# Kernel tuning notes

Hardware: AMD Instinct MI355X
Metric: run time of the kernel (lower is better)

The kernel has to match this reference:

```python
import jax, jax.numpy as jnp
import numpy as np

B, N, C = 16, 1024, 768
E, H, D, K = 8, 192, 4, 2


def setup_inputs() -> dict:
    key = jax.random.key(0)
    ks = jax.random.split(key, 8)
    std = 0.02
    return {
        "x": jax.random.normal(ks[0], (B, N, C), jnp.float32),
        "task_ids": jax.random.randint(ks[1], (B,), 0, D),
        "eps": jax.random.normal(ks[2], (B, N, E), jnp.float32),
        "gate_w": jax.random.normal(ks[3], (D, C, 2 * E), jnp.float32) * std,
        "fc1_w": jax.random.normal(ks[4], (E, H, C), jnp.float32) * std,
        "fc1_b": jnp.zeros((E, H), jnp.float32),
        "fc2_w": jax.random.normal(ks[5], (E, C, H), jnp.float32) * std,
        "fc2_b": jnp.zeros((E, C), jnp.float32),
    }


def reference(x, task_ids, eps, gate_w, fc1_w, fc1_b, fc2_w, fc2_b):
    # per-sample gate selected by domain/task id: [B,N,2E]
    total_w = jnp.einsum("bnc,bce->bne", x, gate_w[task_ids])
    clean_logits, raw_noise = jnp.split(total_w, 2, axis=-1)  # [B,N,E] each
    noise_stddev = jax.nn.softplus(raw_noise) + 0.01
    logits = clean_logits + eps * noise_stddev  # [B,N,E]
    exp_wise_sum = logits.sum(axis=1)  # [B,E]

    top_k_logits, top_k_idx = jax.lax.top_k(exp_wise_sum, K)  # [B,K]
    m1 = top_k_logits.min(axis=1, keepdims=True)
    m2 = top_k_logits.max(axis=1, keepdims=True)
    scaled = (top_k_logits - m1) / (m2 - m1 + 1e-6)
    top_k_gates = jax.nn.softmax(scaled, axis=1)  # [B,K]

    gates_full = jnp.zeros((B, E), x.dtype).at[
        jnp.arange(B)[:, None], top_k_idx
    ].set(top_k_gates)  # [B,E]

    # dense all-expert adapter compute (faithful to original torch.stack)
    h = jnp.einsum("bnc,ehc->benh", x, fc1_w) + fc1_b[None, :, None, :]
    h = jax.nn.gelu(h, approximate=False)
    expert_outs = jnp.einsum("benh,ech->benc", h, fc2_w) + fc2_b[None, :, None, :]

    tot_x = jnp.einsum("be,benc->bnc", gates_full, expert_outs)
    return x + tot_x
```

## Files before the change

### kernel.cpp

```cpp
#include <hip/hip_runtime.h>

#define B_ 16
#define N_ 1024
#define C_ 768
#define E_ 8
#define H_ 192
#define K_ 2

typedef __bf16 bf16x8 __attribute__((ext_vector_type(8)));
typedef float  f32x4  __attribute__((ext_vector_type(4)));

__global__ __launch_bounds__(256) void prep_kernel(
    const float* __restrict__ w1, const float* __restrict__ w2,
    const float* __restrict__ gw,
    __bf16* __restrict__ pw1, __bf16* __restrict__ pw2,
    float* __restrict__ gwT) {
  int idx = blockIdx.x * 256 + threadIdx.x;
  const int nW4 = (E_ * H_ * C_) / 4;
  if (idx >= nW4) return;
  int flat = idx * 4;
  int e = flat / (H_ * C_);
  int r = flat - e * (H_ * C_);

  {
    float4 a = *(const float4*)(w1 + (size_t)flat);
    int n = r / C_;
    int c = r - n * C_;
    size_t o = ((size_t)(e * 24 + (c >> 5)) * 192 + n) * 32 + (c & 31);
    pw1[o + 0] = (__bf16)a.x; pw1[o + 1] = (__bf16)a.y;
    pw1[o + 2] = (__bf16)a.z; pw1[o + 3] = (__bf16)a.w;
  }
  {
    float4 a = *(const float4*)(w2 + (size_t)flat);
    int n = r / H_;
    int h = r - n * H_;
    size_t o = ((size_t)(e * 6 + (h >> 5)) * 768 + n) * 32 + (h & 31);
    pw2[o + 0] = (__bf16)a.x; pw2[o + 1] = (__bf16)a.y;
    pw2[o + 2] = (__bf16)a.z; pw2[o + 3] = (__bf16)a.w;
  }
  if (idx < (4 * 16 * C_) / 4) {
    int f = idx * 4;
    int d = f / (16 * C_);
    int rr = f - d * (16 * C_);
    int j = rr / C_;
    int c = rr - j * C_;
    const float* src = gw + (size_t)d * C_ * 16 + j;
    float4 v;
    v.x = src[(size_t)(c + 0) * 16]; v.y = src[(size_t)(c + 1) * 16];
    v.z = src[(size_t)(c + 2) * 16]; v.w = src[(size_t)(c + 3) * 16];
    *(float4*)(gwT + (size_t)f) = v;
  }
}

__global__ __launch_bounds__(256, 3) void gate_kernel(
    const float* __restrict__ x, const int* __restrict__ task_ids,
    const float* __restrict__ eps, const float* __restrict__ gwT,
    float* __restrict__ sums) {
  const int b = blockIdx.x >> 6;
  const int token0 = (blockIdx.x & 63) * 16;
  const int tid = threadIdx.x;

  __shared__ __align__(16) float xt[16][772];
  __shared__ float sc[16][16];
  __shared__ float red[16][8];

  const float* xbase = x + ((size_t)b * N_ + token0) * C_;
  for (int it = 0; it < 12; ++it) {
    int chunk = it * 256 + tid;
    int row = chunk / 192;
    int col4 = chunk - row * 192;
    float4 v = *(const float4*)(xbase + (size_t)row * C_ + col4 * 4);
    *(float4*)&xt[row][col4 * 4] = v;
  }
  __syncthreads();

  const int t = tid & 15;
  const int j = tid >> 4;
  const int task = task_ids[b];
  const float* wrow = gwT + ((size_t)task * 16 + j) * C_;
  float acc = 0.0f;
#pragma unroll 4
  for (int c = 0; c < C_; c += 4) {
    float4 xv = *(const float4*)&xt[t][c];
    float4 wv = *(const float4*)(wrow + c);
    acc += xv.x * wv.x + xv.y * wv.y + xv.z * wv.z + xv.w * wv.w;
  }
  sc[t][j] = acc;
  __syncthreads();
  if (j < 8) {
    float clean = sc[t][j];
    float raw = sc[t][j + 8];
    float sp = (raw > 20.0f) ? raw : log1pf(expf(raw));
    float lg = clean + eps[((size_t)b * N_ + token0 + t) * E_ + j] * (sp + 0.01f);
    red[t][j] = lg;
  }
  __syncthreads();
  if (tid < 8) {
    float s = 0.0f;
#pragma unroll
    for (int tt = 0; tt < 16; ++tt) s += red[tt][tid];
    atomicAdd(&sums[b * E_ + tid], s);
  }
}

__global__ __launch_bounds__(256, 2) void expert_kernel(
    const float* __restrict__ x, const __bf16* __restrict__ pw1,
    const __bf16* __restrict__ pw2, const float* __restrict__ fc1_b,
    const float* __restrict__ fc2_b, const float* __restrict__ sums,
    float* __restrict__ out) {
  const int b = blockIdx.x >> 5;
  const int token0 = (blockIdx.x & 31) * 32;
  const int tid = threadIdx.x;
  const int wave = tid >> 6;
  const int lane = tid & 63;
  const int ln = lane & 15;
  const int q8 = (lane >> 4) * 8;
  const int q4 = (lane >> 4) * 4;

  __shared__ __align__(16) __bf16 xs[32][776];
  __shared__ __align__(16) __bf16 hs[32][200];

  int e_idx[2]; float gate_v[2];
  {
    const float* s = sums + b * E_;
    float best = -INFINITY, best2 = -INFINITY;
    int i1 = 0, i2 = 0;
#pragma unroll
    for (int e = 0; e < E_; ++e) {
      float v = s[e];
      if (v > best) { best2 = best; i2 = i1; best = v; i1 = e; }
      else if (v > best2) { best2 = v; i2 = e; }
    }
    float d = best - best2;
    float st = d / (d + 1e-6f);
    float et = expf(st);
    e_idx[0] = i1; gate_v[0] = et / (et + 1.0f);
    e_idx[1] = i2; gate_v[1] = 1.0f / (et + 1.0f);
  }

  const float* xbase = x + ((size_t)b * N_ + token0) * C_;
  for (int it = 0; it < 12; ++it) {
    int chunk = it * 256 + tid;
    int row = chunk / 96;
    int col8 = chunk - row * 96;
    const float* p = xbase + (size_t)row * C_ + col8 * 8;
    float4 v0 = *(const float4*)p;
    float4 v1 = *(const float4*)(p + 4);
    bf16x8 t;
    t[0] = (__bf16)v0.x; t[1] = (__bf16)v0.y; t[2] = (__bf16)v0.z; t[3] = (__bf16)v0.w;
    t[4] = (__bf16)v1.x; t[5] = (__bf16)v1.y; t[6] = (__bf16)v1.z; t[7] = (__bf16)v1.w;
    *(bf16x8*)&xs[row][col8 * 8] = t;
  }
  __syncthreads();

  f32x4 c2[2][12] = {};

  for (int kx = 0; kx < 2; ++kx) {
    const int e = e_idx[kx];
    const float g = gate_v[kx];

    const __bf16* w1l = pw1 + (size_t)e * (24 * 192 * 32)
                            + (size_t)(wave * 48 + ln) * 32 + q8;
    bf16x8 bq[2][3], aq[2][2];
#pragma unroll
    for (int j = 0; j < 3; ++j) bq[0][j] = *(const bf16x8*)(w1l + j * 512);
    aq[0][0] = *(const bf16x8*)&xs[ln][q8];
    aq[0][1] = *(const bf16x8*)&xs[16 + ln][q8];
    f32x4 c1[2][3] = {};
#pragma unroll
    for (int kb = 0; kb < 24; ++kb) {
      int p = kb & 1;
      if (kb < 23) {
        const __bf16* nx = w1l + (size_t)(kb + 1) * 6144;
#pragma unroll
        for (int j = 0; j < 3; ++j) bq[p ^ 1][j] = *(const bf16x8*)(nx + j * 512);
        aq[p ^ 1][0] = *(const bf16x8*)&xs[ln][(kb + 1) * 32 + q8];
        aq[p ^ 1][1] = *(const bf16x8*)&xs[16 + ln][(kb + 1) * 32 + q8];
      }
#pragma unroll
      for (int j = 0; j < 3; ++j) {
        c1[0][j] = __builtin_amdgcn_mfma_f32_16x16x32_bf16(aq[p][0], bq[p][j], c1[0][j], 0, 0, 0);
        c1[1][j] = __builtin_amdgcn_mfma_f32_16x16x32_bf16(aq[p][1], bq[p][j], c1[1][j], 0, 0, 0);
      }
    }
#pragma unroll
    for (int j = 0; j < 3; ++j) {
      int col = wave * 48 + j * 16 + ln;
      float b1 = fc1_b[e * H_ + col];
#pragma unroll
      for (int m = 0; m < 2; ++m) {
#pragma unroll
        for (int r = 0; r < 4; ++r) {
          int row = m * 16 + q4 + r;
          float v = c1[m][j][r] + b1;
          float gl = 0.5f * v * (1.0f + erff(v * 0.70710678118f));
          hs[row][col] = (__bf16)(g * gl);
        }
      }
    }
    __syncthreads();

    const __bf16* w2l = pw2 + (size_t)e * (6 * 768 * 32)
                            + (size_t)(wave * 192 + ln) * 32 + q8;
    bf16x8 bh[2][6], av[2][2];
#pragma unroll
    for (int j = 0; j < 6; ++j) bh[0][j] = *(const bf16x8*)(w2l + j * 512);
    av[0][0] = *(const bf16x8*)&hs[ln][q8];
    av[0][1] = *(const bf16x8*)&hs[16 + ln][q8];
#pragma unroll
    for (int s = 0; s < 12; ++s) {
      const int kb = s >> 1;
      const int half = s & 1;
      const int p = s & 1;
      if (s < 11) {
        const int s2 = s + 1;
        const int kb2 = s2 >> 1;
        const int half2 = s2 & 1;
        const __bf16* src = w2l + (size_t)kb2 * 24576;
#pragma unroll
        for (int j = 0; j < 6; ++j)
          bh[p ^ 1][j] = *(const bf16x8*)(src + (half2 * 6 + j) * 512);
        if (half2 == 0) {
          av[kb2 & 1][0] = *(const bf16x8*)&hs[ln][kb2 * 32 + q8];
          av[kb2 & 1][1] = *(const bf16x8*)&hs[16 + ln][kb2 * 32 + q8];
        }
      }
#pragma unroll
      for (int j = 0; j < 6; ++j) {
        const int jj = half * 6 + j;
        c2[0][jj] = __builtin_amdgcn_mfma_f32_16x16x32_bf16(av[kb & 1][0], bh[p][j], c2[0][jj], 0, 0, 0);
        c2[1][jj] = __builtin_amdgcn_mfma_f32_16x16x32_bf16(av[kb & 1][1], bh[p][j], c2[1][jj], 0, 0, 0);
      }
    }
    __syncthreads();
  }

  const float* xr = x + ((size_t)b * N_ + token0) * C_;
  float* outr = out + ((size_t)b * N_ + token0) * C_;
#pragma unroll
  for (int j = 0; j < 12; ++j) {
    int col = wave * 192 + j * 16 + ln;
    float b2t = gate_v[0] * fc2_b[e_idx[0] * C_ + col] +
                gate_v[1] * fc2_b[e_idx[1] * C_ + col];
#pragma unroll
    for (int m = 0; m < 2; ++m) {
#pragma unroll
      for (int r = 0; r < 4; ++r) {
        int row = m * 16 + q4 + r;
        size_t off = (size_t)row * C_ + col;
        outr[off] = xr[off] + c2[m][j][r] + b2t;
      }
    }
  }
}

extern "C" void kernel_launch(void* const* d_in, const int* in_sizes, int n_in,
                              void* d_out, int out_size, void* d_ws, size_t ws_size,
                              hipStream_t stream) {
  const float* x      = (const float*)d_in[0];
  const int*   task   = (const int*)d_in[1];
  const float* eps    = (const float*)d_in[2];
  const float* gate_w = (const float*)d_in[3];
  const float* fc1_w  = (const float*)d_in[4];
  const float* fc1_b  = (const float*)d_in[5];
  const float* fc2_w  = (const float*)d_in[6];
  const float* fc2_b  = (const float*)d_in[7];
  float* out = (float*)d_out;

  const size_t nW = (size_t)E_ * H_ * C_;
  __bf16* pw1 = (__bf16*)d_ws;
  __bf16* pw2 = pw1 + nW;
  float* gwT  = (float*)((char*)d_ws + 2 * nW * sizeof(__bf16));
  float* sums = (float*)((char*)gwT + 4 * 16 * C_ * sizeof(float));

  hipMemsetAsync(sums, 0, B_ * E_ * sizeof(float), stream);
  prep_kernel<<<(nW / 4 + 255) / 256, 256, 0, stream>>>(fc1_w, fc2_w, gate_w,
                                                        pw1, pw2, gwT);
  gate_kernel<<<B_ * 64, 256, 0, stream>>>(x, task, eps, gwT, sums);
  expert_kernel<<<B_ * 32, 256, 0, stream>>>(x, pw1, pw2, fc1_b, fc2_b,
                                             sums, out);
}
```

Baseline: 209.9 us.

## Drop x LDS staging, split fc2 into column halves, raise occupancy

The x tile is no longer converted to bf16 and staged in shared memory. Each wave now loads the fp32 x rows straight from global memory in the fc1 loop and converts them in registers. Both experts' hidden activations are written to a double-sized shared buffer first, so only one barrier is needed, and fc2 then runs in two column halves to halve the accumulator registers. Launch bounds go from 2 to 4 blocks per CU to raise occupancy. In exchange, the four waves each reload x from global/L2 for every expert, rather than reading it once into LDS.

```diff
diff --git a/kernel.cpp b/kernel.cpp
--- a/kernel.cpp
+++ b/kernel.cpp
@@ -103,7 +103,14 @@
   }
 }
 
-__global__ __launch_bounds__(256, 2) void expert_kernel(
+__device__ __forceinline__ bf16x8 cvt8(const float4& a, const float4& b) {
+  bf16x8 t;
+  t[0] = (__bf16)a.x; t[1] = (__bf16)a.y; t[2] = (__bf16)a.z; t[3] = (__bf16)a.w;
+  t[4] = (__bf16)b.x; t[5] = (__bf16)b.y; t[6] = (__bf16)b.z; t[7] = (__bf16)b.w;
+  return t;
+}
+
+__global__ __launch_bounds__(256, 4) void expert_kernel(
     const float* __restrict__ x, const __bf16* __restrict__ pw1,
     const __bf16* __restrict__ pw2, const float* __restrict__ fc1_b,
     const float* __restrict__ fc2_b, const float* __restrict__ sums,
@@ -117,8 +124,7 @@
   const int q8 = (lane >> 4) * 8;
   const int q4 = (lane >> 4) * 4;
 
-  __shared__ __align__(16) __bf16 xs[32][776];
-  __shared__ __align__(16) __bf16 hs[32][200];
+  __shared__ __align__(16) __bf16 hs[2][32][200];
 
   int e_idx[2]; float gate_v[2];
   {
@@ -138,34 +144,24 @@
     e_idx[1] = i2; gate_v[1] = 1.0f / (et + 1.0f);
   }
 
-  const float* xbase = x + ((size_t)b * N_ + token0) * C_;
-  for (int it = 0; it < 12; ++it) {
-    int chunk = it * 256 + tid;
-    int row = chunk / 96;
-    int col8 = chunk - row * 96;
-    const float* p = xbase + (size_t)row * C_ + col8 * 8;
-    float4 v0 = *(const float4*)p;
-    float4 v1 = *(const float4*)(p + 4);
-    bf16x8 t;
-    t[0] = (__bf16)v0.x; t[1] = (__bf16)v0.y; t[2] = (__bf16)v0.z; t[3] = (__bf16)v0.w;
-    t[4] = (__bf16)v1.x; t[5] = (__bf16)v1.y; t[6] = (__bf16)v1.z; t[7] = (__bf16)v1.w;
-    *(bf16x8*)&xs[row][col8 * 8] = t;
-  }
-  __syncthreads();
-
-  f32x4 c2[2][12] = {};
-
+  const float* xrow0 = x + ((size_t)b * N_ + token0 + ln) * C_;
+  const float* xrow1 = xrow0 + 16 * C_;
+
+#pragma unroll
   for (int kx = 0; kx < 2; ++kx) {
     const int e = e_idx[kx];
     const float g = gate_v[kx];
 
     const __bf16* w1l = pw1 + (size_t)e * (24 * 192 * 32)
                             + (size_t)(wave * 48 + ln) * 32 + q8;
-    bf16x8 bq[2][3], aq[2][2];
+    bf16x8 bq[2][3];
+    float4 af[2][2][2];
 #pragma unroll
     for (int j = 0; j < 3; ++j) bq[0][j] = *(const bf16x8*)(w1l + j * 512);
-    aq[0][0] = *(const bf16x8*)&xs[ln][q8];
-    aq[0][1] = *(const bf16x8*)&xs[16 + ln][q8];
+    af[0][0][0] = *(const float4*)(xrow0 + q8);
+    af[0][0][1] = *(const float4*)(xrow0 + q8 + 4);
+    af[0][1][0] = *(const float4*)(xrow1 + q8);
+    af[0][1][1] = *(const float4*)(xrow1 + q8 + 4);
     f32x4 c1[2][3] = {};
 #pragma unroll
     for (int kb = 0; kb < 24; ++kb) {
@@ -174,13 +170,18 @@
         const __bf16* nx = w1l + (size_t)(kb + 1) * 6144;
 #pragma unroll
         for (int j = 0; j < 3; ++j) bq[p ^ 1][j] = *(const bf16x8*)(nx + j * 512);
-        aq[p ^ 1][0] = *(const bf16x8*)&xs[ln][(kb + 1) * 32 + q8];
-        aq[p ^ 1][1] = *(const bf16x8*)&xs[16 + ln][(kb + 1) * 32 + q8];
-      }
+        int ko = (kb + 1) * 32 + q8;
+        af[p ^ 1][0][0] = *(const float4*)(xrow0 + ko);
+        af[p ^ 1][0][1] = *(const float4*)(xrow0 + ko + 4);
+        af[p ^ 1][1][0] = *(const float4*)(xrow1 + ko);
+        af[p ^ 1][1][1] = *(const float4*)(xrow1 + ko + 4);
+      }
+      bf16x8 a0 = cvt8(af[p][0][0], af[p][0][1]);
+      bf16x8 a1 = cvt8(af[p][1][0], af[p][1][1]);
 #pragma unroll
       for (int j = 0; j < 3; ++j) {
-        c1[0][j] = __builtin_amdgcn_mfma_f32_16x16x32_bf16(aq[p][0], bq[p][j], c1[0][j], 0, 0, 0);
-        c1[1][j] = __builtin_amdgcn_mfma_f32_16x16x32_bf16(aq[p][1], bq[p][j], c1[1][j], 0, 0, 0);
+        c1[0][j] = __builtin_amdgcn_mfma_f32_16x16x32_bf16(a0, bq[p][j], c1[0][j], 0, 0, 0);
+        c1[1][j] = __builtin_amdgcn_mfma_f32_16x16x32_bf16(a1, bq[p][j], c1[1][j], 0, 0, 0);
       }
     }
 #pragma unroll
@@ -194,61 +195,70 @@
           int row = m * 16 + q4 + r;
           float v = c1[m][j][r] + b1;
           float gl = 0.5f * v * (1.0f + erff(v * 0.70710678118f));
-          hs[row][col] = (__bf16)(g * gl);
-        }
-      }
-    }
-    __syncthreads();
-
-    const __bf16* w2l = pw2 + (size_t)e * (6 * 768 * 32)
-                            + (size_t)(wave * 192 + ln) * 32 + q8;
-    bf16x8 bh[2][6], av[2][2];
-#pragma unroll
-    for (int j = 0; j < 6; ++j) bh[0][j] = *(const bf16x8*)(w2l + j * 512);
-    av[0][0] = *(const bf16x8*)&hs[ln][q8];
-    av[0][1] = *(const bf16x8*)&hs[16 + ln][q8];
-#pragma unroll
-    for (int s = 0; s < 12; ++s) {
-      const int kb = s >> 1;
-      const int half = s & 1;
-      const int p = s & 1;
-      if (s < 11) {
-        const int s2 = s + 1;
-        const int kb2 = s2 >> 1;
-        const int half2 = s2 & 1;
-        const __bf16* src = w2l + (size_t)kb2 * 24576;
-#pragma unroll
-        for (int j = 0; j < 6; ++j)
-          bh[p ^ 1][j] = *(const bf16x8*)(src + (half2 * 6 + j) * 512);
-        if (half2 == 0) {
-          av[kb2 & 1][0] = *(const bf16x8*)&hs[ln][kb2 * 32 + q8];
-          av[kb2 & 1][1] = *(const bf16x8*)&hs[16 + ln][kb2 * 32 + q8];
-        }
-      }
-#pragma unroll
-      for (int j = 0; j < 6; ++j) {
-        const int jj = half * 6 + j;
-        c2[0][jj] = __builtin_amdgcn_mfma_f32_16x16x32_bf16(av[kb & 1][0], bh[p][j], c2[0][jj], 0, 0, 0);
-        c2[1][jj] = __builtin_amdgcn_mfma_f32_16x16x32_bf16(av[kb & 1][1], bh[p][j], c2[1][jj], 0, 0, 0);
-      }
-    }
-    __syncthreads();
-  }
+          hs[kx][row][col] = (__bf16)(g * gl);
+        }
+      }
+    }
+  }
+  __syncthreads();
 
   const float* xr = x + ((size_t)b * N_ + token0) * C_;
   float* outr = out + ((size_t)b * N_ + token0) * C_;
-#pragma unroll
-  for (int j = 0; j < 12; ++j) {
-    int col = wave * 192 + j * 16 + ln;
-    float b2t = gate_v[0] * fc2_b[e_idx[0] * C_ + col] +
-                gate_v[1] * fc2_b[e_idx[1] * C_ + col];
-#pragma unroll
-    for (int m = 0; m < 2; ++m) {
-#pragma unroll
-      for (int r = 0; r < 4; ++r) {
-        int row = m * 16 + q4 + r;
-        size_t off = (size_t)row * C_ + col;
-        outr[off] = xr[off] + c2[m][j][r] + b2t;
+
+#pragma unroll
+  for (int half = 0; half < 2; ++half) {
+    const int colbase = wave * 192 + half * 96;
+    f32x4 c2[2][6] = {};
+#pragma unroll
+    for (int kx = 0; kx < 2; ++kx) {
+      const int e = e_idx[kx];
+      const __bf16(*hse)[200] = hs[kx];
+      const __bf16* w2l = pw2 + (size_t)e * (6 * 768 * 32)
+                              + (size_t)(colbase + ln) * 32 + q8;
+      bf16x8 bh[2][3], av[2][2];
+#pragma unroll
+      for (int j = 0; j < 3; ++j) bh[0][j] = *(const bf16x8*)(w2l + j * 512);
+      av[0][0] = *(const bf16x8*)&hse[ln][q8];
+      av[0][1] = *(const bf16x8*)&hse[16 + ln][q8];
+#pragma unroll
+      for (int s = 0; s < 12; ++s) {
+        const int kb = s >> 1;
+        const int sub = s & 1;
+        const int p = s & 1;
+        if (s < 11) {
+          const int s2 = s + 1;
+          const int kb2 = s2 >> 1;
+          const int sub2 = s2 & 1;
+          const __bf16* src = w2l + (size_t)kb2 * 24576;
+#pragma unroll
+          for (int j = 0; j < 3; ++j)
+            bh[p ^ 1][j] = *(const bf16x8*)(src + (sub2 * 3 + j) * 512);
+          if (sub2 == 0) {
+            av[kb2 & 1][0] = *(const bf16x8*)&hse[ln][kb2 * 32 + q8];
+            av[kb2 & 1][1] = *(const bf16x8*)&hse[16 + ln][kb2 * 32 + q8];
+          }
+        }
+#pragma unroll
+        for (int j = 0; j < 3; ++j) {
+          const int jj = sub * 3 + j;
+          c2[0][jj] = __builtin_amdgcn_mfma_f32_16x16x32_bf16(av[kb & 1][0], bh[p][j], c2[0][jj], 0, 0, 0);
+          c2[1][jj] = __builtin_amdgcn_mfma_f32_16x16x32_bf16(av[kb & 1][1], bh[p][j], c2[1][jj], 0, 0, 0);
+        }
+      }
+    }
+#pragma unroll
+    for (int j = 0; j < 6; ++j) {
+      int col = colbase + j * 16 + ln;
+      float b2t = gate_v[0] * fc2_b[e_idx[0] * C_ + col] +
+                  gate_v[1] * fc2_b[e_idx[1] * C_ + col];
+#pragma unroll
+      for (int m = 0; m < 2; ++m) {
+#pragma unroll
+        for (int r = 0; r < 4; ++r) {
+          int row = m * 16 + q4 + r;
+          size_t off = (size_t)row * C_ + col;
+          outr[off] = xr[off] + c2[m][j][r] + b2t;
+        }
       }
     }
   }
```

New measurement: 256.2 us. +22.1%, slower.

## Fuse gate and expert kernels into one persistent kernel with grid barrier

Applied to the files above, without the earlier changes.

Merges the gating-reduction kernel and the expert MLP kernel into a single 512-block kernel. Each block first computes gate logits for its 32 tokens, atomically accumulates per-batch expert sums, then waits on a global atomic barrier before selecting the top-2 experts and running the expert compute. The memset is folded into the prep kernel, which zeroes the sums and barrier counter. This removes a launch and a memset and lets the x tile be reread warm from cache. The cost is that the grid barrier depends on all 512 blocks being co-resident (two per CU), or the kernel deadlocks.

```diff
diff --git a/kernel.cpp b/kernel.cpp
--- a/kernel.cpp
+++ b/kernel.cpp
@@ -6,6 +6,7 @@
 #define E_ 8
 #define H_ 192
 #define K_ 2
+#define GRID_ 512
 
 typedef __bf16 bf16x8 __attribute__((ext_vector_type(8)));
 typedef float  f32x4  __attribute__((ext_vector_type(4)));
@@ -14,7 +15,9 @@
     const float* __restrict__ w1, const float* __restrict__ w2,
     const float* __restrict__ gw,
     __bf16* __restrict__ pw1, __bf16* __restrict__ pw2,
-    float* __restrict__ gwT) {
+    float* __restrict__ gwT, unsigned int* __restrict__ ctrl) {
+  if (blockIdx.x == 0 && threadIdx.x < 129) ctrl[threadIdx.x] = 0;
+
   int idx = blockIdx.x * 256 + threadIdx.x;
   const int nW4 = (E_ * H_ * C_) / 4;
   if (idx >= nW4) return;
@@ -52,91 +55,102 @@
   }
 }
 
-__global__ __launch_bounds__(256, 3) void gate_kernel(
+__global__ __launch_bounds__(256, 2) void mega_kernel(
     const float* __restrict__ x, const int* __restrict__ task_ids,
     const float* __restrict__ eps, const float* __restrict__ gwT,
-    float* __restrict__ sums) {
-  const int b = blockIdx.x >> 6;
-  const int token0 = (blockIdx.x & 63) * 16;
+    const __bf16* __restrict__ pw1, const __bf16* __restrict__ pw2,
+    const float* __restrict__ fc1_b, const float* __restrict__ fc2_b,
+    float* __restrict__ sums, unsigned int* __restrict__ bar,
+    float* __restrict__ out) {
+  const int b = blockIdx.x & 15;
+  const int tile = blockIdx.x >> 4;
+  const int token0 = tile * 32;
   const int tid = threadIdx.x;
 
-  __shared__ __align__(16) float xt[16][772];
-  __shared__ float sc[16][16];
-  __shared__ float red[16][8];
-
-  const float* xbase = x + ((size_t)b * N_ + token0) * C_;
-  for (int it = 0; it < 12; ++it) {
-    int chunk = it * 256 + tid;
-    int row = chunk / 192;
-    int col4 = chunk - row * 192;
-    float4 v = *(const float4*)(xbase + (size_t)row * C_ + col4 * 4);
-    *(float4*)&xt[row][col4 * 4] = v;
+  __shared__ __align__(16) char smem[62464];
+  float (*xt)[772]  = (float(*)[772])smem;
+  float (*sc)[16]   = (float(*)[16])(smem + 49408);
+  __bf16 (*xs)[776] = (__bf16(*)[776])smem;
+  __bf16 (*hs)[200] = (__bf16(*)[200])(smem + 49664);
+
+  {
+    const int t = tid & 15;
+    const int jg = tid >> 4;
+    const int task = task_ids[b];
+    const float* wrow = gwT + ((size_t)task * 16 + jg) * C_;
+    float part = 0.0f;
+#pragma unroll
+    for (int pass = 0; pass < 2; ++pass) {
+      const int tb = token0 + pass * 16;
+      const float* xbase = x + ((size_t)b * N_ + tb) * C_;
+      for (int it = 0; it < 12; ++it) {
+        int chunk = it * 256 + tid;
+        int row = chunk / 192;
+        int col4 = chunk - row * 192;
+        *(float4*)&xt[row][col4 * 4] =
+            *(const float4*)(xbase + (size_t)row * C_ + col4 * 4);
+      }
+      __syncthreads();
+      float acc = 0.0f;
+#pragma unroll 4
+      for (int c = 0; c < C_; c += 4) {
+        float4 xv = *(const float4*)&xt[t][c];
+        float4 wv = *(const float4*)(wrow + c);
+        acc += xv.x * wv.x + xv.y * wv.y + xv.z * wv.z + xv.w * wv.w;
+      }
+      sc[t][jg] = acc;
+      __syncthreads();
+      if (jg < 8) {
+        float clean = sc[t][jg];
+        float raw = sc[t][jg + 8];
+        float sp = (raw > 20.0f) ? raw : log1pf(expf(raw));
+        part += clean + eps[((size_t)b * N_ + tb + t) * E_ + jg] * (sp + 0.01f);
+      }
+      __syncthreads();
+    }
+    if (jg < 8) sc[t][jg] = part;
+    __syncthreads();
+    if (tid < 8) {
+      float s = 0.0f;
+#pragma unroll
+      for (int tt = 0; tt < 16; ++tt) s += sc[tt][tid];
+      atomicAdd(&sums[b * E_ + tid], s);
+    }
+    __syncthreads();
+  }
+
+  if (tid == 0) {
+    __threadfence();
+    atomicAdd(bar, 1u);
+    while (__hip_atomic_load(bar, __ATOMIC_ACQUIRE,
+                             __HIP_MEMORY_SCOPE_AGENT) < (unsigned)GRID_)
+      __builtin_amdgcn_s_sleep(8);
   }
   __syncthreads();
 
-  const int t = tid & 15;
-  const int j = tid >> 4;
-  const int task = task_ids[b];
-  const float* wrow = gwT + ((size_t)task * 16 + j) * C_;
-  float acc = 0.0f;
-#pragma unroll 4
-  for (int c = 0; c < C_; c += 4) {
-    float4 xv = *(const float4*)&xt[t][c];
-    float4 wv = *(const float4*)(wrow + c);
-    acc += xv.x * wv.x + xv.y * wv.y + xv.z * wv.z + xv.w * wv.w;
-  }
-  sc[t][j] = acc;
-  __syncthreads();
-  if (j < 8) {
-    float clean = sc[t][j];
-    float raw = sc[t][j + 8];
-    float sp = (raw > 20.0f) ? raw : log1pf(expf(raw));
-    float lg = clean + eps[((size_t)b * N_ + token0 + t) * E_ + j] * (sp + 0.01f);
-    red[t][j] = lg;
-  }
-  __syncthreads();
-  if (tid < 8) {
-    float s = 0.0f;
-#pragma unroll
-    for (int tt = 0; tt < 16; ++tt) s += red[tt][tid];
-    atomicAdd(&sums[b * E_ + tid], s);
-  }
-}
-
-__global__ __launch_bounds__(256, 2) void expert_kernel(
-    const float* __restrict__ x, const __bf16* __restrict__ pw1,
-    const __bf16* __restrict__ pw2, const float* __restrict__ fc1_b,
-    const float* __restrict__ fc2_b, const float* __restrict__ sums,
-    float* __restrict__ out) {
-  const int b = blockIdx.x >> 5;
-  const int token0 = (blockIdx.x & 31) * 32;
-  const int tid = threadIdx.x;
+  int e_idx[2]; float gate_v[2];
+  {
+    float best = -INFINITY, best2 = -INFINITY;
+    int i1 = 0, i2 = 0;
+#pragma unroll
+    for (int e = 0; e < E_; ++e) {
+      float v = __hip_atomic_load(&sums[b * E_ + e], __ATOMIC_RELAXED,
+                                  __HIP_MEMORY_SCOPE_AGENT);
+      if (v > best) { best2 = best; i2 = i1; best = v; i1 = e; }
+      else if (v > best2) { best2 = v; i2 = e; }
+    }
+    float d = best - best2;
+    float st = d / (d + 1e-6f);
+    float et = expf(st);
+    e_idx[0] = i1; gate_v[0] = et / (et + 1.0f);
+    e_idx[1] = i2; gate_v[1] = 1.0f / (et + 1.0f);
+  }
+
   const int wave = tid >> 6;
   const int lane = tid & 63;
   const int ln = lane & 15;
   const int q8 = (lane >> 4) * 8;
   const int q4 = (lane >> 4) * 4;
-
-  __shared__ __align__(16) __bf16 xs[32][776];
-  __shared__ __align__(16) __bf16 hs[32][200];
-
-  int e_idx[2]; float gate_v[2];
-  {
-    const float* s = sums + b * E_;
-    float best = -INFINITY, best2 = -INFINITY;
-    int i1 = 0, i2 = 0;
-#pragma unroll
-    for (int e = 0; e < E_; ++e) {
-      float v = s[e];
-      if (v > best) { best2 = best; i2 = i1; best = v; i1 = e; }
-      else if (v > best2) { best2 = v; i2 = e; }
-    }
-    float d = best - best2;
-    float st = d / (d + 1e-6f);
-    float et = expf(st);
-    e_idx[0] = i1; gate_v[0] = et / (et + 1.0f);
-    e_idx[1] = i2; gate_v[1] = 1.0f / (et + 1.0f);
-  }
 
   const float* xbase = x + ((size_t)b * N_ + token0) * C_;
   for (int it = 0; it < 12; ++it) {
@@ -272,11 +286,10 @@
   __bf16* pw2 = pw1 + nW;
   float* gwT  = (float*)((char*)d_ws + 2 * nW * sizeof(__bf16));
   float* sums = (float*)((char*)gwT + 4 * 16 * C_ * sizeof(float));
-
-  hipMemsetAsync(sums, 0, B_ * E_ * sizeof(float), stream);
-  prep_kernel<<<(nW / 4 + 255) / 256, 256, 0, stream>>>(fc1_w, fc2_w, gate_w,
-                                                        pw1, pw2, gwT);
-  gate_kernel<<<B_ * 64, 256, 0, stream>>>(x, task, eps, gwT, sums);
-  expert_kernel<<<B_ * 32, 256, 0, stream>>>(x, pw1, pw2, fc1_b, fc2_b,
-                                             sums, out);
+  unsigned int* bar = (unsigned int*)(sums + 128);
+
+  prep_kernel<<<(nW / 4 + 255) / 256, 256, 0, stream>>>(
+      fc1_w, fc2_w, gate_w, pw1, pw2, gwT, (unsigned int*)sums);
+  mega_kernel<<<GRID_, 256, 0, stream>>>(x, task, eps, gwT, pw1, pw2,
+                                         fc1_b, fc2_b, sums, bar, out);
 }
```

Result: slower. 237.0 us (+12.9%).
